# Optimization experiments

Hardware: AMD Instinct MI355X
Metric: run time of the kernel (lower is better)

The kernel has to match this reference:

```python
import jax, jax.numpy as jnp
import numpy as np

# Faithful GCN forward (eval mode, dropout = identity).
# GraphConvolution(x, adj): adj @ (x @ W) + b
# GraphConvolution_edge(edge_feat, adj): edge_feat = cat(x_i, x_j) over all (i,j) pairs,
#   support = edge_feat @ W  (shape [N*N, H]), out[i] = sum_j adj[i,j] * support[i,j] + b.
# materialized: out = (x @ W_top) * rowsum(adj)[:, None] + adj @ (x @ W_bot) + b.

N, NFEAT, NHID = 1536, 512, 64

def _edge_conv(x, adj, W, b):
    H = x.shape[-1]
    A = x @ W[:H]          # [N, H] contribution of x_i
    B = x @ W[H:]          # [N, H] contribution of x_j
    deg = jnp.sum(adj, axis=1, keepdims=True)  # [N, 1]
    return A * deg + adj @ B + b


def setup_inputs() -> dict:
    key = jax.random.key(0)
    ks = jax.random.split(key, 10)
    s1 = 1.0 / np.sqrt(NFEAT)
    s2 = 1.0 / np.sqrt(2 * NHID)
    return {
        "x_init": jax.random.normal(ks[0], (N, NFEAT), jnp.float32),
        "adj": jax.random.uniform(ks[1], (N, N), jnp.float32) / N,
        "adj1": jax.random.uniform(ks[2], (N, N), jnp.float32) / N,
        "fully_connected_graph": jnp.ones((N, N), jnp.float32),
        "W1": jax.random.uniform(ks[3], (NFEAT, NHID), jnp.float32, -s1, s1),
        "b1": jax.random.uniform(ks[4], (NHID,), jnp.float32, -s1, s1),
        "W2": jax.random.uniform(ks[5], (2 * NHID, NHID), jnp.float32, -s2, s2),
        "b2": jax.random.uniform(ks[6], (NHID,), jnp.float32, -s2, s2),
        "W3": jax.random.uniform(ks[7], (2 * NHID, NHID), jnp.float32, -s2, s2),
        "b3": jax.random.uniform(ks[8], (NHID,), jnp.float32, -s2, s2),
    }


def reference(x_init, adj, adj1, fully_connected_graph, W1, b1, W2, b2, W3, b3):
    # gc1: node graph conv + relu (dropout is identity in eval)
    x = jax.nn.relu(adj1 @ (x_init @ W1) + b1)          # [N, NHID]
    # gc_e2: pairwise edge conv + elu
    x = jax.nn.elu(_edge_conv(x, adj1, W2, b2))          # [N, NHID]
    # gc_e3: pairwise edge conv (no activation)
    x = _edge_conv(x, adj1, W3, b3)                      # [N, NHID]
    return jax.nn.log_softmax(x, axis=1)
```

## Files before the change

### kernel.cpp

```cpp
#include <hip/hip_runtime.h>
#include <cmath>

constexpr int NN   = 1536;
constexpr int FF   = 512;
constexpr int HH   = 64;
constexpr int RPB  = 16;
constexpr int NB   = NN / RPB;
constexpr int NT   = 1024;
constexpr int WAVES = NT / 64;
constexpr int KST  = NN / 32;
constexpr int KST1 = FF / 32;

using f32x4  = __attribute__((ext_vector_type(4))) float;
using bf16x8 = __attribute__((ext_vector_type(8))) short;
typedef unsigned short u16;

__device__ __forceinline__ u16 f2bf(float f) {
  unsigned u = __builtin_bit_cast(unsigned, f);
  return (u16)((u + 0x7fffu + ((u >> 16) & 1u)) >> 16);
}


__global__ __launch_bounds__(NT, 4) void k_pre(
    const float* __restrict__ x, const float* __restrict__ adj,
    const float* __restrict__ W1,
    u16* __restrict__ adjT, u16* __restrict__ t1T, float* __restrict__ deg) {
  __shared__ u16 Al[KST1 * 512];
  __shared__ u16 Bl[KST1 * 4 * 512];
  __shared__ u16 Jl[KST * 512];
  __shared__ float red[4][4][16][16];
  const int tid = threadIdx.x, lane = tid & 63, wave = tid >> 6;
  const int i0 = blockIdx.x * RPB;

  {
    int i = tid >> 6, j0 = (tid & 63) * 8;
    const float* src = x + (size_t)(i0 + i) * FF + j0;
    bf16x8 v;
#pragma unroll
    for (int jj = 0; jj < 8; ++jj) v[jj] = (short)f2bf(src[jj]);
    *(bf16x8*)&Al[(j0 >> 5) * 512 + ((j0 & 31) >> 3) * 128 + i * 8] = v;
  }
  {
    int k = tid >> 1, c0 = (tid & 1) * 32;
    const float* src = W1 + (size_t)k * HH + c0;
    int base = (k >> 5) * 4 * 512 + ((k & 31) >> 3) * 128 + (k & 7);
    for (int cc = 0; cc < 32; ++cc) {
      int c = c0 + cc;
      Bl[base + (c >> 4) * 512 + (c & 15) * 8] = f2bf(src[cc]);
    }
  }
  {
    int i = tid >> 6, j0 = (tid & 63) * 24;
    const float* src = adj + (size_t)(i0 + i) * NN + j0;
    float dsum = 0.f;
#pragma unroll
    for (int g = 0; g < 3; ++g) {
      bf16x8 v;
#pragma unroll
      for (int jj = 0; jj < 8; ++jj) {
        float f = src[g * 8 + jj];
        dsum += f;
        v[jj] = (short)f2bf(f);
      }
      int k = j0 + g * 8;
      *(bf16x8*)&Jl[(k >> 5) * 512 + ((k & 31) >> 3) * 128 + i * 8] = v;
    }
#pragma unroll
    for (int off = 32; off; off >>= 1) dsum += __shfl_xor(dsum, off, 64);
    if ((tid & 63) == 0) deg[i0 + i] = dsum;
  }
  __syncthreads();

  {
    const float4* srcv = (const float4*)Jl;
    float4* dstv = (float4*)(adjT + (size_t)blockIdx.x * KST * 512);
#pragma unroll
    for (int s = 0; s < 3; ++s) dstv[tid + s * NT] = srcv[tid + s * NT];
  }
  {
    const int ks = wave >> 2, cg = wave & 3;
    f32x4 acc = {0.f, 0.f, 0.f, 0.f};
#pragma unroll
    for (int s = 0; s < 4; ++s) {
      int t = ks * 4 + s;
      bf16x8 a = *(const bf16x8*)&Al[t * 512 + lane * 8];
      bf16x8 b = *(const bf16x8*)&Bl[(t * 4 + cg) * 512 + lane * 8];
      acc = __builtin_amdgcn_mfma_f32_16x16x32_bf16(a, b, acc, 0, 0, 0);
    }
#pragma unroll
    for (int q = 0; q < 4; ++q)
      red[ks][cg][(lane >> 4) * 4 + q][lane & 15] = acc[q];
  }
  __syncthreads();
  {
    int r = tid >> 6, c = tid & 63;
    float v = red[0][c >> 4][r][c & 15] + red[1][c >> 4][r][c & 15] +
              red[2][c >> 4][r][c & 15] + red[3][c >> 4][r][c & 15];
    int k = i0 + r;
    t1T[((k >> 5) * 4 + (c >> 4)) * 512 + ((k & 31) >> 3) * 128 +
        (c & 15) * 8 + (k & 7)] = f2bf(v);
  }
}

template <int MODE>
__global__ __launch_bounds__(NT, 4) void k_layer(
    const u16* __restrict__ adjT, const u16* __restrict__ TT,
    const float* __restrict__ Ain, const float* __restrict__ deg,
    const float* __restrict__ bias, const float* __restrict__ Wn,
    float* __restrict__ outA, u16* __restrict__ outBT,
    float* __restrict__ out) {
  __shared__ float red[WAVES][4][16][16];
  __shared__ float xloc[16][HH];
  __shared__ float Wl[2 * HH * HH];
  const int tid = threadIdx.x, lane = tid & 63, wave = tid >> 6;
  const int i0 = blockIdx.x * RPB;

  if (MODE < 2) {
    const float4* src = (const float4*)Wn;
    float4* dst = (float4*)Wl;
    for (int idx = tid; idx < 2 * HH * HH / 4; idx += NT) dst[idx] = src[idx];
  }

  const u16* ja = adjT + (size_t)blockIdx.x * KST * 512;
  bf16x8 a[3], b[3][4];
#pragma unroll
  for (int s = 0; s < 3; ++s) {
    int kstep = wave * 3 + s;
    a[s] = *(const bf16x8*)(ja + kstep * 512 + lane * 8);
#pragma unroll
    for (int cg = 0; cg < 4; ++cg)
      b[s][cg] = *(const bf16x8*)(TT + (size_t)(kstep * 4 + cg) * 512 + lane * 8);
  }
  f32x4 acc[4] = {{0,0,0,0},{0,0,0,0},{0,0,0,0},{0,0,0,0}};
#pragma unroll
  for (int s = 0; s < 3; ++s)
#pragma unroll
    for (int cg = 0; cg < 4; ++cg)
      acc[cg] = __builtin_amdgcn_mfma_f32_16x16x32_bf16(a[s], b[s][cg], acc[cg], 0, 0, 0);
#pragma unroll
  for (int cg = 0; cg < 4; ++cg)
#pragma unroll
    for (int q = 0; q < 4; ++q)
      red[wave][cg][(lane >> 4) * 4 + q][lane & 15] = acc[cg][q];
  __syncthreads();

  {
    int r = tid >> 6, c = tid & 63;
    float v = bias[c];
#pragma unroll
    for (int w = 0; w < WAVES; ++w) v += red[w][c >> 4][r][c & 15];
    if (MODE >= 1) v += Ain[(size_t)(i0 + r) * HH + c] * deg[i0 + r];
    if (MODE == 0) v = fmaxf(v, 0.f);
    if (MODE == 1) v = v > 0.f ? v : expm1f(v);
    xloc[r][c] = v;
  }
  __syncthreads();

  if (MODE < 2) {
#pragma unroll
    for (int t = 0; t < 2; ++t) {
      int idx = tid + t * NT;
      int r = idx >> 7, cc = idx & 127, half = cc >> 6, col = cc & 63;
      float sacc = 0.f;
#pragma unroll
      for (int k = 0; k < HH; ++k)
        sacc = fmaf(xloc[r][k], Wl[(half * HH + k) * HH + col], sacc);
      if (half == 0) {
        outA[(size_t)(i0 + r) * HH + col] = sacc;
      } else {
        int kk = i0 + r;
        outBT[((kk >> 5) * 4 + (col >> 4)) * 512 + ((kk & 31) >> 3) * 128 +
              (col & 15) * 8 + (kk & 7)] = f2bf(sacc);
      }
    }
  } else {
    int r = wave;
    float v = xloc[r][lane];
    float m = v;
#pragma unroll
    for (int off = 32; off; off >>= 1) m = fmaxf(m, __shfl_xor(m, off, 64));
    float e = expf(v - m);
    float ssum = e;
#pragma unroll
    for (int off = 32; off; off >>= 1) ssum += __shfl_xor(ssum, off, 64);
    out[(size_t)(i0 + r) * HH + lane] = v - m - logf(ssum);
  }
}

extern "C" void kernel_launch(void* const* d_in, const int* in_sizes, int n_in,
                              void* d_out, int out_size, void* d_ws,
                              size_t ws_size, hipStream_t stream) {
  const float* x   = (const float*)d_in[0];
  const float* adj = (const float*)d_in[2];
  const float* W1  = (const float*)d_in[4];
  const float* b1  = (const float*)d_in[5];
  const float* W2  = (const float*)d_in[6];
  const float* b2  = (const float*)d_in[7];
  const float* W3  = (const float*)d_in[8];
  const float* b3  = (const float*)d_in[9];
  float* out = (float*)d_out;

  char* ws = (char*)d_ws;
  u16* adjT = (u16*)ws;
  u16* t1T  = (u16*)(ws + 4718592);
  u16* B2T  = (u16*)(ws + 4915200);
  u16* B3T  = (u16*)(ws + 5111808);
  float* A2 = (float*)(ws + 5308416);
  float* A3 = (float*)(ws + 5701632);
  float* dg = (float*)(ws + 6094848);

  k_pre<<<NB, NT, 0, stream>>>(x, adj, W1, adjT, t1T, dg);
  k_layer<0><<<NB, NT, 0, stream>>>(adjT, t1T, nullptr, dg, b1, W2, A2, B2T, nullptr);
  k_layer<1><<<NB, NT, 0, stream>>>(adjT, B2T, A2, dg, b2, W3, A3, B3T, nullptr);
  k_layer<2><<<NB, NT, 0, stream>>>(adjT, B3T, A3, dg, b3, nullptr, nullptr, nullptr, out);
}
```

Before: 33.85 us.

## Fuse all GCN layers into one cooperative kernel with grid barriers

Replaces the four kernel launches with a single cooperative kernel that synchronises layers through an atomic grid barrier. Each block keeps its adjacency row slice (bf16), degrees and the per-row A term in shared memory, so adjT, A2/A3 and deg are no longer written to and re-read from global memory. This removes launch gaps and global round-trips. In exchange it adds spin-wait barriers, a memset launch, and a large shared-memory footprint that could limit residency; the grid of 96 blocks must be co-resident.

```diff
diff --git a/kernel.cpp b/kernel.cpp
--- a/kernel.cpp
+++ b/kernel.cpp
@@ -1,15 +1,15 @@
 #include <hip/hip_runtime.h>
 #include <cmath>
 
-constexpr int NN   = 1536;
-constexpr int FF   = 512;
-constexpr int HH   = 64;
-constexpr int RPB  = 16;
-constexpr int NB   = NN / RPB;
-constexpr int NT   = 1024;
+constexpr int NN    = 1536;
+constexpr int FF    = 512;
+constexpr int HH    = 64;
+constexpr int RPB   = 16;
+constexpr int NB    = NN / RPB;
+constexpr int NT    = 1024;
 constexpr int WAVES = NT / 64;
-constexpr int KST  = NN / 32;
-constexpr int KST1 = FF / 32;
+constexpr int KST   = NN / 32;
+constexpr int KST1  = FF / 32;
 
 using f32x4  = __attribute__((ext_vector_type(4))) float;
 using bf16x8 = __attribute__((ext_vector_type(8))) short;
@@ -20,65 +20,89 @@
   return (u16)((u + 0x7fffu + ((u >> 16) & 1u)) >> 16);
 }
 
-
-__global__ __launch_bounds__(NT, 4) void k_pre(
-    const float* __restrict__ x, const float* __restrict__ adj,
-    const float* __restrict__ W1,
-    u16* __restrict__ adjT, u16* __restrict__ t1T, float* __restrict__ deg) {
-  __shared__ u16 Al[KST1 * 512];
-  __shared__ u16 Bl[KST1 * 4 * 512];
-  __shared__ u16 Jl[KST * 512];
-  __shared__ float red[4][4][16][16];
+struct Params {
+  const float *x, *adj, *W1, *b1, *W2, *b2, *W3, *b3;
+  u16 *t1T, *B2T, *B3T;
+  float* out;
+  unsigned* bar;
+};
+
+__device__ __forceinline__ void gbar(unsigned* c, unsigned target) {
+  __syncthreads();
+  if (threadIdx.x == 0) {
+    __hip_atomic_fetch_add(c, 1u, __ATOMIC_RELEASE, __HIP_MEMORY_SCOPE_AGENT);
+    while (__hip_atomic_load(c, __ATOMIC_RELAXED, __HIP_MEMORY_SCOPE_AGENT) <
+           target)
+      __builtin_amdgcn_s_sleep(4);
+    __hip_atomic_fetch_add(c, 0u, __ATOMIC_ACQUIRE, __HIP_MEMORY_SCOPE_AGENT);
+  }
+  __syncthreads();
+}
+
+
+__global__ __launch_bounds__(NT, 4) void gcn_all(Params p) {
+  __shared__ u16 adjL[KST * 512];
+  __shared__ __attribute__((aligned(16))) char uni[96 * 1024];
+  __shared__ float xloc[RPB][HH];
+  __shared__ float anext[RPB][HH];
+  __shared__ float degs[RPB];
+
+  u16*   Al   = (u16*)uni;
+  u16*   Bl   = (u16*)(uni + 16 * 1024);
+  float* red0 = (float*)(uni + 80 * 1024);
+  float* Wl   = (float*)uni;
+  float* red  = (float*)(uni + 32 * 1024);
+
   const int tid = threadIdx.x, lane = tid & 63, wave = tid >> 6;
   const int i0 = blockIdx.x * RPB;
 
   {
-    int i = tid >> 6, j0 = (tid & 63) * 8;
-    const float* src = x + (size_t)(i0 + i) * FF + j0;
+    int j0 = lane * 8;
+    const float* src = p.x + (size_t)(i0 + wave) * FF + j0;
     bf16x8 v;
 #pragma unroll
     for (int jj = 0; jj < 8; ++jj) v[jj] = (short)f2bf(src[jj]);
-    *(bf16x8*)&Al[(j0 >> 5) * 512 + ((j0 & 31) >> 3) * 128 + i * 8] = v;
+    *(bf16x8*)&Al[(j0 >> 5) * 512 + ((j0 & 31) >> 3) * 128 + wave * 8] = v;
   }
   {
     int k = tid >> 1, c0 = (tid & 1) * 32;
-    const float* src = W1 + (size_t)k * HH + c0;
-    int base = (k >> 5) * 4 * 512 + ((k & 31) >> 3) * 128 + (k & 7);
-    for (int cc = 0; cc < 32; ++cc) {
-      int c = c0 + cc;
-      Bl[base + (c >> 4) * 512 + (c & 15) * 8] = f2bf(src[cc]);
-    }
-  }
-  {
-    int i = tid >> 6, j0 = (tid & 63) * 24;
-    const float* src = adj + (size_t)(i0 + i) * NN + j0;
-    float dsum = 0.f;
+    const float4* src = (const float4*)(p.W1 + (size_t)k * HH + c0);
+    int base = (k >> 5) * 2048 + ((k & 31) >> 3) * 128 + (k & 7);
+#pragma unroll
+    for (int g = 0; g < 8; ++g) {
+      float4 f = src[g];
+      int c = c0 + g * 4;
+      int off = base + (c >> 4) * 512 + (c & 15) * 8;
+      Bl[off]      = f2bf(f.x);
+      Bl[off + 8]  = f2bf(f.y);
+      Bl[off + 16] = f2bf(f.z);
+      Bl[off + 24] = f2bf(f.w);
+    }
+  }
+  {
+    int j0 = lane * 24;
+    const float* src = p.adj + (size_t)(i0 + wave) * NN + j0;
+    float ds = 0.f;
 #pragma unroll
     for (int g = 0; g < 3; ++g) {
       bf16x8 v;
 #pragma unroll
       for (int jj = 0; jj < 8; ++jj) {
         float f = src[g * 8 + jj];
-        dsum += f;
+        ds += f;
         v[jj] = (short)f2bf(f);
       }
       int k = j0 + g * 8;
-      *(bf16x8*)&Jl[(k >> 5) * 512 + ((k & 31) >> 3) * 128 + i * 8] = v;
-    }
-#pragma unroll
-    for (int off = 32; off; off >>= 1) dsum += __shfl_xor(dsum, off, 64);
-    if ((tid & 63) == 0) deg[i0 + i] = dsum;
-  }
-  __syncthreads();
-
-  {
-    const float4* srcv = (const float4*)Jl;
-    float4* dstv = (float4*)(adjT + (size_t)blockIdx.x * KST * 512);
-#pragma unroll
-    for (int s = 0; s < 3; ++s) dstv[tid + s * NT] = srcv[tid + s * NT];
-  }
-  {
-    const int ks = wave >> 2, cg = wave & 3;
+      *(bf16x8*)&adjL[(k >> 5) * 512 + ((k & 31) >> 3) * 128 + wave * 8] = v;
+    }
+#pragma unroll
+    for (int off = 32; off; off >>= 1) ds += __shfl_xor(ds, off, 64);
+    if (lane == 0) degs[wave] = ds;
+  }
+  __syncthreads();
+
+  {
+    int ks = wave >> 2, cg = wave & 3;
     f32x4 acc = {0.f, 0.f, 0.f, 0.f};
 #pragma unroll
     for (int s = 0; s < 4; ++s) {
@@ -89,128 +113,135 @@
     }
 #pragma unroll
     for (int q = 0; q < 4; ++q)
-      red[ks][cg][(lane >> 4) * 4 + q][lane & 15] = acc[q];
-  }
-  __syncthreads();
-  {
-    int r = tid >> 6, c = tid & 63;
-    float v = red[0][c >> 4][r][c & 15] + red[1][c >> 4][r][c & 15] +
-              red[2][c >> 4][r][c & 15] + red[3][c >> 4][r][c & 15];
+      red0[((ks * 4 + cg) * 16 + ((lane >> 4) * 4 + q)) * 16 + (lane & 15)] =
+          acc[q];
+  }
+  __syncthreads();
+  {
+    int r = wave, c = lane;
+    float v = 0.f;
+#pragma unroll
+    for (int ks2 = 0; ks2 < 4; ++ks2)
+      v += red0[((ks2 * 4 + (c >> 4)) * 16 + r) * 16 + (c & 15)];
     int k = i0 + r;
-    t1T[((k >> 5) * 4 + (c >> 4)) * 512 + ((k & 31) >> 3) * 128 +
-        (c & 15) * 8 + (k & 7)] = f2bf(v);
-  }
-}
-
-template <int MODE>
-__global__ __launch_bounds__(NT, 4) void k_layer(
-    const u16* __restrict__ adjT, const u16* __restrict__ TT,
-    const float* __restrict__ Ain, const float* __restrict__ deg,
-    const float* __restrict__ bias, const float* __restrict__ Wn,
-    float* __restrict__ outA, u16* __restrict__ outBT,
-    float* __restrict__ out) {
-  __shared__ float red[WAVES][4][16][16];
-  __shared__ float xloc[16][HH];
-  __shared__ float Wl[2 * HH * HH];
-  const int tid = threadIdx.x, lane = tid & 63, wave = tid >> 6;
-  const int i0 = blockIdx.x * RPB;
-
-  if (MODE < 2) {
-    const float4* src = (const float4*)Wn;
+    p.t1T[((k >> 5) * 4 + (c >> 4)) * 512 + ((k & 31) >> 3) * 128 +
+          (c & 15) * 8 + (k & 7)] = f2bf(v);
+  }
+  __syncthreads();
+  {
+    const float4* src = (const float4*)p.W2;
     float4* dst = (float4*)Wl;
-    for (int idx = tid; idx < 2 * HH * HH / 4; idx += NT) dst[idx] = src[idx];
-  }
-
-  const u16* ja = adjT + (size_t)blockIdx.x * KST * 512;
-  bf16x8 a[3], b[3][4];
-#pragma unroll
-  for (int s = 0; s < 3; ++s) {
-    int kstep = wave * 3 + s;
-    a[s] = *(const bf16x8*)(ja + kstep * 512 + lane * 8);
+#pragma unroll
+    for (int s = 0; s < 2; ++s) dst[tid + s * NT] = src[tid + s * NT];
+  }
+  gbar(p.bar, NB);
+
+#pragma unroll 1
+  for (int l = 0; l < 3; ++l) {
+    const u16* TT    = l == 0 ? p.t1T : (l == 1 ? p.B2T : p.B3T);
+    const float* bia = l == 0 ? p.b1 : (l == 1 ? p.b2 : p.b3);
+    u16* Bout        = l == 0 ? p.B2T : p.B3T;
+
+    bf16x8 a[3], b[3][4];
+#pragma unroll
+    for (int s = 0; s < 3; ++s) {
+      int kst = wave * 3 + s;
+      a[s] = *(const bf16x8*)&adjL[kst * 512 + lane * 8];
+#pragma unroll
+      for (int cg = 0; cg < 4; ++cg)
+        b[s][cg] =
+            *(const bf16x8*)(TT + (size_t)(kst * 4 + cg) * 512 + lane * 8);
+    }
+    f32x4 acc[4] = {{0, 0, 0, 0}, {0, 0, 0, 0}, {0, 0, 0, 0}, {0, 0, 0, 0}};
+#pragma unroll
+    for (int s = 0; s < 3; ++s)
+#pragma unroll
+      for (int cg = 0; cg < 4; ++cg)
+        acc[cg] =
+            __builtin_amdgcn_mfma_f32_16x16x32_bf16(a[s], b[s][cg], acc[cg], 0, 0, 0);
 #pragma unroll
     for (int cg = 0; cg < 4; ++cg)
-      b[s][cg] = *(const bf16x8*)(TT + (size_t)(kstep * 4 + cg) * 512 + lane * 8);
-  }
-  f32x4 acc[4] = {{0,0,0,0},{0,0,0,0},{0,0,0,0},{0,0,0,0}};
-#pragma unroll
-  for (int s = 0; s < 3; ++s)
-#pragma unroll
-    for (int cg = 0; cg < 4; ++cg)
-      acc[cg] = __builtin_amdgcn_mfma_f32_16x16x32_bf16(a[s], b[s][cg], acc[cg], 0, 0, 0);
-#pragma unroll
-  for (int cg = 0; cg < 4; ++cg)
-#pragma unroll
-    for (int q = 0; q < 4; ++q)
-      red[wave][cg][(lane >> 4) * 4 + q][lane & 15] = acc[cg][q];
-  __syncthreads();
-
-  {
-    int r = tid >> 6, c = tid & 63;
-    float v = bias[c];
-#pragma unroll
-    for (int w = 0; w < WAVES; ++w) v += red[w][c >> 4][r][c & 15];
-    if (MODE >= 1) v += Ain[(size_t)(i0 + r) * HH + c] * deg[i0 + r];
-    if (MODE == 0) v = fmaxf(v, 0.f);
-    if (MODE == 1) v = v > 0.f ? v : expm1f(v);
-    xloc[r][c] = v;
-  }
-  __syncthreads();
-
-  if (MODE < 2) {
-#pragma unroll
-    for (int t = 0; t < 2; ++t) {
-      int idx = tid + t * NT;
-      int r = idx >> 7, cc = idx & 127, half = cc >> 6, col = cc & 63;
-      float sacc = 0.f;
-#pragma unroll
-      for (int k = 0; k < HH; ++k)
-        sacc = fmaf(xloc[r][k], Wl[(half * HH + k) * HH + col], sacc);
-      if (half == 0) {
-        outA[(size_t)(i0 + r) * HH + col] = sacc;
-      } else {
-        int kk = i0 + r;
-        outBT[((kk >> 5) * 4 + (col >> 4)) * 512 + ((kk & 31) >> 3) * 128 +
-              (col & 15) * 8 + (kk & 7)] = f2bf(sacc);
+#pragma unroll
+      for (int q = 0; q < 4; ++q)
+        red[((wave * 4 + cg) * 16 + ((lane >> 4) * 4 + q)) * 16 + (lane & 15)] =
+            acc[cg][q];
+    __syncthreads();
+
+    {
+      int r = wave, c = lane;
+      float v = bia[c];
+#pragma unroll
+      for (int w = 0; w < WAVES; ++w)
+        v += red[((w * 4 + (c >> 4)) * 16 + r) * 16 + (c & 15)];
+      if (l >= 1) v += anext[r][c] * degs[r];
+      if (l == 0) v = fmaxf(v, 0.f);
+      if (l == 1) v = v > 0.f ? v : expm1f(v);
+      xloc[r][c] = v;
+    }
+    __syncthreads();
+
+    if (l < 2) {
+#pragma unroll
+      for (int t = 0; t < 2; ++t) {
+        int idx = tid + t * NT;
+        int r = idx >> 7, cc = idx & 127, half = cc >> 6, col = cc & 63;
+        float s = 0.f;
+#pragma unroll
+        for (int k = 0; k < HH; ++k)
+          s = fmaf(xloc[r][k], Wl[(half * HH + k) * HH + col], s);
+        if (half == 0) {
+          anext[r][col] = s;
+        } else {
+          int kk = i0 + r;
+          Bout[((kk >> 5) * 4 + (col >> 4)) * 512 + ((kk & 31) >> 3) * 128 +
+               (col & 15) * 8 + (kk & 7)] = f2bf(s);
+        }
       }
-    }
-  } else {
-    int r = wave;
-    float v = xloc[r][lane];
-    float m = v;
-#pragma unroll
-    for (int off = 32; off; off >>= 1) m = fmaxf(m, __shfl_xor(m, off, 64));
-    float e = expf(v - m);
-    float ssum = e;
-#pragma unroll
-    for (int off = 32; off; off >>= 1) ssum += __shfl_xor(ssum, off, 64);
-    out[(size_t)(i0 + r) * HH + lane] = v - m - logf(ssum);
+      __syncthreads();
+      if (l == 0) {
+        const float4* src = (const float4*)p.W3;
+        float4* dst = (float4*)Wl;
+#pragma unroll
+        for (int s2 = 0; s2 < 2; ++s2) dst[tid + s2 * NT] = src[tid + s2 * NT];
+      }
+      gbar(p.bar, (unsigned)((2 + l) * NB));
+    } else {
+      float v = xloc[wave][lane];
+      float m = v;
+#pragma unroll
+      for (int off = 32; off; off >>= 1) m = fmaxf(m, __shfl_xor(m, off, 64));
+      float e = expf(v - m);
+      float ssum = e;
+#pragma unroll
+      for (int off = 32; off; off >>= 1) ssum += __shfl_xor(ssum, off, 64);
+      p.out[(size_t)(i0 + wave) * HH + lane] = v - m - logf(ssum);
+    }
   }
 }
 
 extern "C" void kernel_launch(void* const* d_in, const int* in_sizes, int n_in,
                               void* d_out, int out_size, void* d_ws,
                               size_t ws_size, hipStream_t stream) {
-  const float* x   = (const float*)d_in[0];
-  const float* adj = (const float*)d_in[2];
-  const float* W1  = (const float*)d_in[4];
-  const float* b1  = (const float*)d_in[5];
-  const float* W2  = (const float*)d_in[6];
-  const float* b2  = (const float*)d_in[7];
-  const float* W3  = (const float*)d_in[8];
-  const float* b3  = (const float*)d_in[9];
-  float* out = (float*)d_out;
+  Params p;
+  p.x   = (const float*)d_in[0];
+  p.adj = (const float*)d_in[2];
+  p.W1  = (const float*)d_in[4];
+  p.b1  = (const float*)d_in[5];
+  p.W2  = (const float*)d_in[6];
+  p.b2  = (const float*)d_in[7];
+  p.W3  = (const float*)d_in[8];
+  p.b3  = (const float*)d_in[9];
+  p.out = (float*)d_out;
 
   char* ws = (char*)d_ws;
-  u16* adjT = (u16*)ws;
-  u16* t1T  = (u16*)(ws + 4718592);
-  u16* B2T  = (u16*)(ws + 4915200);
-  u16* B3T  = (u16*)(ws + 5111808);
-  float* A2 = (float*)(ws + 5308416);
-  float* A3 = (float*)(ws + 5701632);
-  float* dg = (float*)(ws + 6094848);
-
-  k_pre<<<NB, NT, 0, stream>>>(x, adj, W1, adjT, t1T, dg);
-  k_layer<0><<<NB, NT, 0, stream>>>(adjT, t1T, nullptr, dg, b1, W2, A2, B2T, nullptr);
-  k_layer<1><<<NB, NT, 0, stream>>>(adjT, B2T, A2, dg, b2, W3, A3, B3T, nullptr);
-  k_layer<2><<<NB, NT, 0, stream>>>(adjT, B3T, A3, dg, b3, nullptr, nullptr, nullptr, out);
-}
+  p.t1T = (u16*)ws;
+  p.B2T = (u16*)(ws + 196608);
+  p.B3T = (u16*)(ws + 393216);
+  p.bar = (unsigned*)(ws + 589824);
+
+  hipMemsetAsync((void*)p.bar, 0, 128, stream);
+
+  void* args[] = {&p};
+  hipLaunchCooperativeKernel((const void*)gcn_all, dim3(NB), dim3(NT), args, 0,
+                             stream);
+}
```

Measured after the change: 65.21 us. 92.6% more time.

## Stage B operand via LDS DMA, MFMA next-layer projection, new B layout

Applied to the files above, without the earlier changes.

The layer kernel now streams the shared B operand (T^T) into LDS in two halves with global_load_lds, and reads fragments from there instead of holding all B fragments in registers. The per-row projection by the next layer's weights switches from a scalar FMA loop over fp32 LDS to bf16 MFMA, with the weights packed into an MFMA-friendly layout. The cross-wave reduction is halved to 8 slots in a padded buffer, and the B-matrix layout is changed through a new bidx helper. This aims to cut register pressure and scalar ALU work, but it adds a large LDS footprint (~152KB) that limits occupancy to one block per CU and adds extra bf16 rounding in the projection.

```diff
diff --git a/kernel.cpp b/kernel.cpp
--- a/kernel.cpp
+++ b/kernel.cpp
@@ -7,12 +7,12 @@
 constexpr int RPB  = 16;
 constexpr int NB   = NN / RPB;
 constexpr int NT   = 1024;
-constexpr int WAVES = NT / 64;
 constexpr int KST  = NN / 32;
 constexpr int KST1 = FF / 32;
 
 using f32x4  = __attribute__((ext_vector_type(4))) float;
 using bf16x8 = __attribute__((ext_vector_type(8))) short;
+using u16x4  = __attribute__((ext_vector_type(4))) unsigned short;
 typedef unsigned short u16;
 
 __device__ __forceinline__ u16 f2bf(float f) {
@@ -20,6 +20,27 @@
   return (u16)((u + 0x7fffu + ((u >> 16) & 1u)) >> 16);
 }
 
+__device__ __forceinline__ size_t bidx(int k, int c) {
+  return (size_t)((c >> 5) * (KST * 2) + (k >> 5) * 2 + ((c >> 4) & 1)) * 512 +
+         ((k & 31) >> 3) * 128 + (c & 15) * 8 + (k & 7);
+}
+
+__device__ __forceinline__ void gl_lds16(const void* g, void* l) {
+  __builtin_amdgcn_global_load_lds(
+      (const __attribute__((address_space(1))) unsigned*)g,
+      (__attribute__((address_space(3))) unsigned*)l, 16, 0, 0);
+}
+
+__device__ __forceinline__ void pack_wnb(u16* WnB, const float* Wsrc, int tid) {
+  int jp = tid & 127, kb = (tid >> 7) * 8;
+  int srow0 = (jp >> 6) * 64, col = jp & 63;
+#pragma unroll
+  for (int i = 0; i < 8; ++i) {
+    int k = kb + i;
+    WnB[((k >> 5) * 8 + (jp >> 4)) * 512 + ((k & 31) >> 3) * 128 +
+        (jp & 15) * 8 + (k & 7)] = f2bf(Wsrc[(size_t)(srow0 + k) * HH + col]);
+  }
+}
 
 __global__ __launch_bounds__(NT, 4) void k_pre(
     const float* __restrict__ x, const float* __restrict__ adj,
@@ -28,46 +49,47 @@
   __shared__ u16 Al[KST1 * 512];
   __shared__ u16 Bl[KST1 * 4 * 512];
   __shared__ u16 Jl[KST * 512];
-  __shared__ float red[4][4][16][16];
+  __shared__ float red0[4][4][16][16];
   const int tid = threadIdx.x, lane = tid & 63, wave = tid >> 6;
   const int i0 = blockIdx.x * RPB;
 
   {
-    int i = tid >> 6, j0 = (tid & 63) * 8;
-    const float* src = x + (size_t)(i0 + i) * FF + j0;
+    int j0 = lane * 8;
+    const float* src = x + (size_t)(i0 + wave) * FF + j0;
     bf16x8 v;
 #pragma unroll
     for (int jj = 0; jj < 8; ++jj) v[jj] = (short)f2bf(src[jj]);
-    *(bf16x8*)&Al[(j0 >> 5) * 512 + ((j0 & 31) >> 3) * 128 + i * 8] = v;
+    *(bf16x8*)&Al[(j0 >> 5) * 512 + ((j0 & 31) >> 3) * 128 + wave * 8] = v;
   }
   {
     int k = tid >> 1, c0 = (tid & 1) * 32;
     const float* src = W1 + (size_t)k * HH + c0;
-    int base = (k >> 5) * 4 * 512 + ((k & 31) >> 3) * 128 + (k & 7);
+    int base = (k >> 5) * 2048 + ((k & 31) >> 3) * 128 + (k & 7);
+#pragma unroll 8
     for (int cc = 0; cc < 32; ++cc) {
       int c = c0 + cc;
       Bl[base + (c >> 4) * 512 + (c & 15) * 8] = f2bf(src[cc]);
     }
   }
   {
-    int i = tid >> 6, j0 = (tid & 63) * 24;
-    const float* src = adj + (size_t)(i0 + i) * NN + j0;
-    float dsum = 0.f;
+    int j0 = lane * 24;
+    const float* src = adj + (size_t)(i0 + wave) * NN + j0;
+    float ds = 0.f;
 #pragma unroll
     for (int g = 0; g < 3; ++g) {
       bf16x8 v;
 #pragma unroll
       for (int jj = 0; jj < 8; ++jj) {
         float f = src[g * 8 + jj];
-        dsum += f;
+        ds += f;
         v[jj] = (short)f2bf(f);
       }
       int k = j0 + g * 8;
-      *(bf16x8*)&Jl[(k >> 5) * 512 + ((k & 31) >> 3) * 128 + i * 8] = v;
-    }
-#pragma unroll
-    for (int off = 32; off; off >>= 1) dsum += __shfl_xor(dsum, off, 64);
-    if ((tid & 63) == 0) deg[i0 + i] = dsum;
+      *(bf16x8*)&Jl[(k >> 5) * 512 + ((k & 31) >> 3) * 128 + wave * 8] = v;
+    }
+#pragma unroll
+    for (int off = 32; off; off >>= 1) ds += __shfl_xor(ds, off, 64);
+    if (lane == 0) deg[i0 + wave] = ds;
   }
   __syncthreads();
 
@@ -78,7 +100,7 @@
     for (int s = 0; s < 3; ++s) dstv[tid + s * NT] = srcv[tid + s * NT];
   }
   {
-    const int ks = wave >> 2, cg = wave & 3;
+    int ks = wave >> 2, cg = wave & 3;
     f32x4 acc = {0.f, 0.f, 0.f, 0.f};
 #pragma unroll
     for (int s = 0; s < 4; ++s) {
@@ -89,16 +111,14 @@
     }
 #pragma unroll
     for (int q = 0; q < 4; ++q)
-      red[ks][cg][(lane >> 4) * 4 + q][lane & 15] = acc[q];
-  }
-  __syncthreads();
-  {
-    int r = tid >> 6, c = tid & 63;
-    float v = red[0][c >> 4][r][c & 15] + red[1][c >> 4][r][c & 15] +
-              red[2][c >> 4][r][c & 15] + red[3][c >> 4][r][c & 15];
-    int k = i0 + r;
-    t1T[((k >> 5) * 4 + (c >> 4)) * 512 + ((k & 31) >> 3) * 128 +
-        (c & 15) * 8 + (k & 7)] = f2bf(v);
+      red0[ks][cg][(lane >> 4) * 4 + q][lane & 15] = acc[q];
+  }
+  __syncthreads();
+  {
+    int r = wave, c = lane;
+    float v = red0[0][c >> 4][r][c & 15] + red0[1][c >> 4][r][c & 15] +
+              red0[2][c >> 4][r][c & 15] + red0[3][c >> 4][r][c & 15];
+    t1T[bidx(i0 + r, c)] = f2bf(v);
   }
 }
 
@@ -109,73 +129,108 @@
     const float* __restrict__ bias, const float* __restrict__ Wn,
     float* __restrict__ outA, u16* __restrict__ outBT,
     float* __restrict__ out) {
-  __shared__ float red[WAVES][4][16][16];
-  __shared__ float xloc[16][HH];
-  __shared__ float Wl[2 * HH * HH];
+  __shared__ __attribute__((aligned(16))) char LB[155712];
+  float* red8 = (float*)(LB + 98304);
+  u16*   WnB  = (u16*)(LB + 133120);
+  u16*   xA   = (u16*)(LB + 149504);
+  float* xloc = (float*)(LB + 151552);
+
   const int tid = threadIdx.x, lane = tid & 63, wave = tid >> 6;
   const int i0 = blockIdx.x * RPB;
 
-  if (MODE < 2) {
-    const float4* src = (const float4*)Wn;
-    float4* dst = (float4*)Wl;
-    for (int idx = tid; idx < 2 * HH * HH / 4; idx += NT) dst[idx] = src[idx];
-  }
-
-  const u16* ja = adjT + (size_t)blockIdx.x * KST * 512;
-  bf16x8 a[3], b[3][4];
-#pragma unroll
-  for (int s = 0; s < 3; ++s) {
-    int kstep = wave * 3 + s;
-    a[s] = *(const bf16x8*)(ja + kstep * 512 + lane * 8);
+  const u16* ja = adjT + (size_t)blockIdx.x * (KST * 512);
+  bf16x8 afr[3];
+#pragma unroll
+  for (int s = 0; s < 3; ++s)
+    afr[s] = *(const bf16x8*)(ja + (wave * 3 + s) * 512 + lane * 8);
+
+  if (MODE < 2) pack_wnb(WnB, Wn, tid);
+  float dg = 0.f;
+  if (MODE >= 1) dg = deg[i0 + wave];
+
+  f32x4 acc[4] = {{0, 0, 0, 0}, {0, 0, 0, 0}, {0, 0, 0, 0}, {0, 0, 0, 0}};
+#pragma unroll
+  for (int h = 0; h < 2; ++h) {
+    {
+      const char* gsrc = (const char*)TT + (size_t)h * 98304 + wave * 6144 +
+                         (size_t)lane * 16;
+      char* ldst = LB + wave * 6144;
+      asm volatile("s_waitcnt lgkmcnt(0)" ::: "memory");
+#pragma unroll
+      for (int r = 0; r < 6; ++r) gl_lds16(gsrc + r * 1024, ldst + r * 1024);
+    }
+    asm volatile("s_waitcnt vmcnt(0)" ::: "memory");
+    __builtin_amdgcn_sched_barrier(0);
+#pragma unroll
+    for (int s = 0; s < 3; ++s)
+#pragma unroll
+      for (int chi = 0; chi < 2; ++chi) {
+        bf16x8 b = *(const bf16x8*)(LB + wave * 6144 + (s * 2 + chi) * 1024 +
+                                    lane * 16);
+        acc[h * 2 + chi] = __builtin_amdgcn_mfma_f32_16x16x32_bf16(
+            afr[s], b, acc[h * 2 + chi], 0, 0, 0);
+      }
+  }
+
+  if (wave < 8) {
 #pragma unroll
     for (int cg = 0; cg < 4; ++cg)
-      b[s][cg] = *(const bf16x8*)(TT + (size_t)(kstep * 4 + cg) * 512 + lane * 8);
-  }
-  f32x4 acc[4] = {{0,0,0,0},{0,0,0,0},{0,0,0,0},{0,0,0,0}};
-#pragma unroll
-  for (int s = 0; s < 3; ++s)
+#pragma unroll
+      for (int q = 0; q < 4; ++q)
+        red8[((wave * 4 + cg) * 16 + ((lane >> 4) * 4 + q)) * 17 +
+             (lane & 15)] = acc[cg][q];
+  }
+  __syncthreads();
+  if (wave >= 8) {
 #pragma unroll
     for (int cg = 0; cg < 4; ++cg)
-      acc[cg] = __builtin_amdgcn_mfma_f32_16x16x32_bf16(a[s], b[s][cg], acc[cg], 0, 0, 0);
-#pragma unroll
-  for (int cg = 0; cg < 4; ++cg)
-#pragma unroll
-    for (int q = 0; q < 4; ++q)
-      red[wave][cg][(lane >> 4) * 4 + q][lane & 15] = acc[cg][q];
-  __syncthreads();
-
-  {
-    int r = tid >> 6, c = tid & 63;
-    float v = bias[c];
-#pragma unroll
-    for (int w = 0; w < WAVES; ++w) v += red[w][c >> 4][r][c & 15];
-    if (MODE >= 1) v += Ain[(size_t)(i0 + r) * HH + c] * deg[i0 + r];
+#pragma unroll
+      for (int q = 0; q < 4; ++q)
+        red8[(((wave - 8) * 4 + cg) * 16 + ((lane >> 4) * 4 + q)) * 17 +
+             (lane & 15)] += acc[cg][q];
+  }
+  __syncthreads();
+
+  {
+    float v = bias[lane];
+#pragma unroll
+    for (int s = 0; s < 8; ++s)
+      v += red8[((s * 4 + (lane >> 4)) * 16 + wave) * 17 + (lane & 15)];
+    if (MODE >= 1) v += Ain[(size_t)(i0 + wave) * HH + lane] * dg;
     if (MODE == 0) v = fmaxf(v, 0.f);
     if (MODE == 1) v = v > 0.f ? v : expm1f(v);
-    xloc[r][c] = v;
+    xloc[wave * 65 + lane] = v;
+    if (MODE < 2)
+      xA[(lane >> 5) * 512 + ((lane & 31) >> 3) * 128 + wave * 8 +
+         (lane & 7)] = f2bf(v);
   }
   __syncthreads();
 
   if (MODE < 2) {
-#pragma unroll
-    for (int t = 0; t < 2; ++t) {
-      int idx = tid + t * NT;
-      int r = idx >> 7, cc = idx & 127, half = cc >> 6, col = cc & 63;
-      float sacc = 0.f;
-#pragma unroll
-      for (int k = 0; k < HH; ++k)
-        sacc = fmaf(xloc[r][k], Wl[(half * HH + k) * HH + col], sacc);
-      if (half == 0) {
-        outA[(size_t)(i0 + r) * HH + col] = sacc;
+    if (wave < 8) {
+      f32x4 a2 = {0.f, 0.f, 0.f, 0.f};
+#pragma unroll
+      for (int s = 0; s < 2; ++s) {
+        bf16x8 a = *(const bf16x8*)&xA[s * 512 + lane * 8];
+        bf16x8 b = *(const bf16x8*)&WnB[(s * 8 + wave) * 512 + lane * 8];
+        a2 = __builtin_amdgcn_mfma_f32_16x16x32_bf16(a, b, a2, 0, 0, 0);
+      }
+      int row = (lane >> 4) * 4, colg = lane & 15;
+      if (wave < 4) {
+        int c = wave * 16 + colg;
+#pragma unroll
+        for (int q = 0; q < 4; ++q)
+          outA[(size_t)(i0 + row + q) * HH + c] = a2[q];
       } else {
-        int kk = i0 + r;
-        outBT[((kk >> 5) * 4 + (col >> 4)) * 512 + ((kk & 31) >> 3) * 128 +
-              (col & 15) * 8 + (kk & 7)] = f2bf(sacc);
+        int c = (wave - 4) * 16 + colg;
+        u16x4 v;
+#pragma unroll
+        for (int q = 0; q < 4; ++q) v[q] = f2bf(a2[q]);
+        *(u16x4*)&outBT[bidx(i0 + row, c)] = v;
       }
     }
   } else {
-    int r = wave;
-    float v = xloc[r][lane];
+    float v = xloc[wave * 65 + lane];
     float m = v;
 #pragma unroll
     for (int off = 32; off; off >>= 1) m = fmaxf(m, __shfl_xor(m, off, 64));
@@ -183,7 +238,7 @@
     float ssum = e;
 #pragma unroll
     for (int off = 32; off; off >>= 1) ssum += __shfl_xor(ssum, off, 64);
-    out[(size_t)(i0 + r) * HH + lane] = v - m - logf(ssum);
+    out[(size_t)(i0 + wave) * HH + lane] = v - m - logf(ssum);
   }
 }
 
@@ -210,7 +265,10 @@
   float* dg = (float*)(ws + 6094848);
 
   k_pre<<<NB, NT, 0, stream>>>(x, adj, W1, adjT, t1T, dg);
-  k_layer<0><<<NB, NT, 0, stream>>>(adjT, t1T, nullptr, dg, b1, W2, A2, B2T, nullptr);
-  k_layer<1><<<NB, NT, 0, stream>>>(adjT, B2T, A2, dg, b2, W3, A3, B3T, nullptr);
-  k_layer<2><<<NB, NT, 0, stream>>>(adjT, B3T, A3, dg, b3, nullptr, nullptr, nullptr, out);
-}
+  k_layer<0><<<NB, NT, 0, stream>>>(adjT, t1T, nullptr, nullptr, b1, W2, A2,
+                                    B2T, nullptr);
+  k_layer<1><<<NB, NT, 0, stream>>>(adjT, B2T, A2, dg, b2, W3, A3, B3T,
+                                    nullptr);
+  k_layer<2><<<NB, NT, 0, stream>>>(adjT, B3T, A3, dg, b3, nullptr, nullptr,
+                                    nullptr, out);
+}
```

Result: faster. 30.28 us (-10.6%).
